# Optimization experiments

Measured on AMD Instinct MI355X. Metric: run time of the kernel, lower is better.

The kernel has to match this reference:

```python
import jax, jax.numpy as jnp
import numpy as np

B, S = 1024, 512
V, E, H, T = 50000, 300, 800, 50


def setup_inputs() -> dict:
    key = jax.random.key(0)
    ks = jax.random.split(key, 8)
    ids = jax.random.randint(ks[0], (B, S), 0, V, dtype=jnp.int64 if jax.config.jax_enable_x64 else jnp.int32)
    return {
        "ids": ids,
        "rho": jax.random.normal(ks[1], (V, E), jnp.float32) * 0.02,
        "alpha": jax.random.normal(ks[2], (T, E), jnp.float32) * 0.02,
        "W1": jax.random.normal(ks[3], (E, H), jnp.float32) * 0.05,
        "b1": jnp.zeros((H,), jnp.float32),
        "Wmu": jax.random.normal(ks[4], (H, T), jnp.float32) * 0.05,
        "bmu": jnp.zeros((T,), jnp.float32),
        "Wlv": jax.random.normal(ks[5], (H, T), jnp.float32) * 0.05,
        "blv": jnp.zeros((T,), jnp.float32),
    }


def reference(ids, rho, alpha, W1, b1, Wmu, bmu, Wlv, blv):
    b, s = ids.shape
    v = rho.shape[0]
    # bag-of-words histogram: scatter-add instead of dense one_hot+reduce_sum
    bows = jnp.zeros((b, v), rho.dtype).at[jnp.arange(b)[:, None], ids].add(1.0)
    # zero out special tokens 1 and 2 (original: x * (1 - sum(one_hot([1,2]))))
    bows = bows.at[:, jnp.array([1, 2])].set(0.0)
    normal_bows = bows / jnp.sum(bows, axis=-1, keepdims=True)
    # encoder (eval mode: dropout is identity)
    x = jnp.einsum('bv,ve->be', normal_bows, rho)
    h = jax.nn.relu(x @ W1 + b1)
    mu_theta = h @ Wmu + bmu
    logsigma_theta = h @ Wlv + blv
    kl_theta = -0.5 * jnp.sum(1.0 + logsigma_theta - mu_theta**2 - jnp.exp(logsigma_theta), axis=-1)
    # reparameterize (eval/inference mode): z = mu
    theta = jax.nn.softmax(mu_theta, axis=-1)  # [B, T]
    beta = jax.nn.softmax(jnp.einsum('te,ve->tv', alpha, rho), axis=-1)  # [T, V]
    lookup = jnp.log(theta @ beta + 1e-5)  # [B, V]
    recon_loss = -jnp.sum(lookup * bows, axis=-1)
    loss = jnp.mean(recon_loss) + jnp.mean(kl_theta)
    return theta, loss
```

## Files before the change

kernel.cpp:

```cpp
#include <hip/hip_runtime.h>
#include <math.h>


#define Bn 1024
#define Sn 512
#define Vn 50000
#define En 300
#define Hn 800
#define Tn 50
#define KP 320
#define BSTR 64
#define W1FRAG_N (50 * 10 * 64 * 8)
#define WFRAG_N  (8 * 25 * 64 * 8)
#define NRANGE 8
#define VRANGE (Vn / NRANGE)

typedef __bf16 bf16x8 __attribute__((ext_vector_type(8)));
typedef float  f32x4  __attribute__((ext_vector_type(4)));

__device__ __forceinline__ float waveReduceSum(float v) {
    #pragma unroll
    for (int off = 32; off > 0; off >>= 1) v += __shfl_xor(v, off, 64);
    return v;
}
__device__ __forceinline__ float waveReduceMax(float v) {
    #pragma unroll
    for (int off = 32; off > 0; off >>= 1) v = fmaxf(v, __shfl_xor(v, off, 64));
    return v;
}
__device__ __forceinline__ unsigned short f2bf(float x) {
    unsigned u = __float_as_uint(x);
    return (unsigned short)((u + 0x7FFFu + ((u >> 16) & 1u)) >> 16);
}
__device__ __forceinline__ float bf_lo(unsigned u) { return __uint_as_float(u << 16); }
__device__ __forceinline__ float bf_hi(unsigned u) { return __uint_as_float(u & 0xFFFF0000u); }

__global__ __launch_bounds__(256) void k0_init(
        const float* __restrict__ alpha, const float* __restrict__ W1,
        const float* __restrict__ Wmu, const float* __restrict__ Wlv,
        unsigned short* __restrict__ bfrag, unsigned short* __restrict__ w1frag,
        unsigned short* __restrict__ wfrag, float* __restrict__ topicsumR,
        float* __restrict__ loss, float* __restrict__ xbar) {
    const int gid = blockIdx.x * 256 + threadIdx.x;
    if (gid < 512) topicsumR[gid] = 0.f;
    if (gid == 520) *loss = 0.f;
    if (gid < Bn * En) xbar[gid] = 0.f;
    if (gid < 4 * 10 * 64 * 8) {
        int j = gid & 7;
        int lane = (gid >> 3) & 63;
        int rest = gid >> 9;
        int kt = rest % 10, w = rest / 10;
        int t = 16 * w + (lane & 15);
        int e = kt * 32 + (lane >> 4) * 8 + j;
        bfrag[gid] = (t < Tn && e < En) ? f2bf(alpha[t * En + e]) : (unsigned short)0;
    }
    if (gid < W1FRAG_N) {
        int j = gid & 7, lane = (gid >> 3) & 63, rest = gid >> 9;
        int kt = rest % 10, nt = rest / 10;
        int e = kt * 32 + (lane >> 4) * 8 + j;
        int hcol = nt * 16 + (lane & 15);
        w1frag[gid] = (e < En) ? f2bf(W1[e * Hn + hcol]) : (unsigned short)0;
    } else {
        int g2 = gid - W1FRAG_N;
        if (g2 < WFRAG_N) {
            int j = g2 & 7, lane = (g2 >> 3) & 63, rest = g2 >> 9;
            int kt = rest % 25, nt = rest / 25;
            int k = kt * 32 + (lane >> 4) * 8 + j;
            int t = (nt & 3) * 16 + (lane & 15);
            float val = 0.f;
            if (t < Tn) val = (nt < 4) ? Wmu[k * Tn + t] : Wlv[k * Tn + t];
            wfrag[g2] = f2bf(val);
        }
    }
}

__global__ __launch_bounds__(256) void k5_cast(
        const float4* __restrict__ rho4, ushort4* __restrict__ rhoh4) {
    const int i = blockIdx.x * 256 + threadIdx.x;
    if (i < Vn * (KP / 4)) {
        int v = i / (KP / 4), s = i - v * (KP / 4);
        ushort4 p = {0, 0, 0, 0};
        if (s < En / 4) {
            float4 r = rho4[v * (En / 4) + s];
            p.x = f2bf(r.x); p.y = f2bf(r.y); p.z = f2bf(r.z); p.w = f2bf(r.w);
        }
        rhoh4[i] = p;
    }
}

__global__ __launch_bounds__(256) void k4_beta(
        const unsigned short* __restrict__ rhoh,
        const unsigned short* __restrict__ bfrag,
        unsigned int* __restrict__ betaU32, float* __restrict__ topicsumR) {
    __shared__ unsigned short trans[16 * 66];
    const int tid = threadIdx.x;
    const int wave = tid >> 6, lane = tid & 63;
    const int quad = lane >> 4, l15 = lane & 15;
    const int v0 = blockIdx.x * 16;

    const unsigned short* arow = rhoh + (size_t)(v0 + l15) * KP + quad * 8;
    f32x4 acc = {0.f, 0.f, 0.f, 0.f};
    #pragma unroll
    for (int kt = 0; kt < 10; ++kt) {
        bf16x8 a = *(const bf16x8*)(arow + kt * 32);
        bf16x8 bv = *(const bf16x8*)(bfrag + ((wave * 10 + kt) * 64 + lane) * 8);
        acc = __builtin_amdgcn_mfma_f32_16x16x32_bf16(a, bv, acc, 0, 0, 0);
    }
    float ts = 0.f;
    #pragma unroll
    for (int r = 0; r < 4; ++r) {
        float ev = expf(acc[r]);
        ts += ev;
        trans[(quad * 4 + r) * 66 + 16 * wave + l15] = f2bf(ev);
    }
    ts += __shfl_xor(ts, 16, 64);
    ts += __shfl_xor(ts, 32, 64);
    const int t = 16 * wave + l15;
    if (lane < 16 && t < Tn)
        atomicAdd(&topicsumR[(blockIdx.x & 7) * 64 + t], ts);
    __syncthreads();
    unsigned int* dst = betaU32 + (size_t)v0 * 32;
    const unsigned int* tr32 = (const unsigned int*)trans;
    for (int i = tid; i < 16 * 32; i += 256)
        dst[i] = tr32[(i >> 5) * 33 + (i & 31)];
}

__global__ __launch_bounds__(256) void k1_tokens_x(
        const int* __restrict__ ids, const unsigned int* __restrict__ rhoh32,
        int* __restrict__ toks, int* __restrict__ cnt,
        float* __restrict__ xbar) {
    __shared__ int sid[Sn];
    __shared__ int sfid[Sn];
    __shared__ int scount, sfull;
    const int blk = blockIdx.x;
    const int r = blk & (NRANGE - 1), b = blk >> 3;
    const int tid = threadIdx.x;
    const int lo = r * VRANGE, hi = lo + VRANGE;
    if (tid == 0) { scount = 0; sfull = 0; }
    __syncthreads();
    #pragma unroll
    for (int s0 = 0; s0 < Sn; s0 += 256) {
        int id = ids[b * Sn + s0 + tid];
        bool val = (id != 1 && id != 2);
        if (val && id >= lo && id < hi) {
            int p = atomicAdd(&scount, 1);
            sid[p] = id;
        }
        if (r == 0 && val) {
            int p = atomicAdd(&sfull, 1);
            sfid[p] = id;
        }
    }
    __syncthreads();
    if (r == 0) {
        const int nf = sfull;
        for (int i = tid; i < nf; i += 256) toks[b * Sn + i] = sfid[i];
        if (tid == 0) cnt[b] = nf;
    }
    const int m = scount;
    if (tid < En / 2 && m > 0) {
        float ax = 0.f, ay = 0.f;
        for (int s = 0; s < m; ++s) {
            unsigned u = rhoh32[sid[s] * (KP / 2) + tid];
            ax += bf_lo(u);
            ay += bf_hi(u);
        }
        atomicAdd(&xbar[b * En + 2 * tid], ax);
        atomicAdd(&xbar[b * En + 2 * tid + 1], ay);
    }
}

__global__ __launch_bounds__(256) void k2a_xcast(
        const float* __restrict__ xbar, const int* __restrict__ cnt,
        unsigned short* __restrict__ xbh) {
    const int gid = blockIdx.x * 256 + threadIdx.x;
    if (gid < Bn * KP) {
        int b = gid / KP, e = gid - b * KP;
        unsigned short out = 0;
        if (e < En) {
            float invn = 1.0f / (float)cnt[b];
            out = f2bf(xbar[b * En + e] * invn);
        }
        xbh[gid] = out;
    }
}

__global__ __launch_bounds__(256) void k2_h(
        const unsigned short* __restrict__ xbh,
        const unsigned short* __restrict__ w1frag,
        const float* __restrict__ b1, unsigned short* __restrict__ hbh) {
    const int tid = threadIdx.x;
    const int wave = tid >> 6, lane = tid & 63;
    const int quad = lane >> 4, l15 = lane & 15;
    const int b0 = blockIdx.x * 16;
    const int nt = blockIdx.y * 4 + wave;
    if (nt >= 50) return;
    const unsigned short* arow = xbh + (size_t)(b0 + l15) * KP + quad * 8;
    f32x4 acc = {0.f, 0.f, 0.f, 0.f};
    #pragma unroll
    for (int kt = 0; kt < 10; ++kt) {
        bf16x8 a = *(const bf16x8*)(arow + kt * 32);
        bf16x8 bv = *(const bf16x8*)(w1frag + ((size_t)(nt * 10 + kt) * 64 + lane) * 8);
        acc = __builtin_amdgcn_mfma_f32_16x16x32_bf16(a, bv, acc, 0, 0, 0);
    }
    const int col = nt * 16 + l15;
    const float bias = b1[col];
    #pragma unroll
    for (int r = 0; r < 4; ++r) {
        int row = b0 + quad * 4 + r;
        hbh[(size_t)row * Hn + col] = f2bf(fmaxf(acc[r] + bias, 0.f));
    }
}

__global__ __launch_bounds__(256) void k3_theta(
        const unsigned short* __restrict__ hbh,
        const unsigned short* __restrict__ wfrag,
        const float* __restrict__ bmu, const float* __restrict__ blv,
        float* __restrict__ theta, float* __restrict__ loss) {
    __shared__ float mlds[16 * 65];
    __shared__ float llds[16 * 65];
    const int tid = threadIdx.x;
    const int wave = tid >> 6, lane = tid & 63;
    const int quad = lane >> 4, l15 = lane & 15;
    const int b0 = blockIdx.x * 16;
    const unsigned short* arow = hbh + (size_t)(b0 + l15) * Hn + quad * 8;
    f32x4 am = {0.f, 0.f, 0.f, 0.f}, al = {0.f, 0.f, 0.f, 0.f};
    #pragma unroll
    for (int kt = 0; kt < 25; ++kt) {
        bf16x8 a  = *(const bf16x8*)(arow + kt * 32);
        bf16x8 bm = *(const bf16x8*)(wfrag + ((size_t)(wave * 25 + kt) * 64 + lane) * 8);
        bf16x8 bl = *(const bf16x8*)(wfrag + ((size_t)((4 + wave) * 25 + kt) * 64 + lane) * 8);
        am = __builtin_amdgcn_mfma_f32_16x16x32_bf16(a, bm, am, 0, 0, 0);
        al = __builtin_amdgcn_mfma_f32_16x16x32_bf16(a, bl, al, 0, 0, 0);
    }
    const int t = wave * 16 + l15;
    const float bm_ = (t < Tn) ? bmu[t] : 0.f;
    const float bl_ = (t < Tn) ? blv[t] : 0.f;
    #pragma unroll
    for (int r = 0; r < 4; ++r) {
        int row = quad * 4 + r;
        mlds[row * 65 + t] = am[r] + bm_;
        llds[row * 65 + t] = al[r] + bl_;
    }
    __syncthreads();
    const int tt = (lane < Tn) ? lane : (Tn - 1);
    const bool act = (lane < Tn);
    float klacc = 0.f;
    #pragma unroll
    for (int k = 0; k < 4; ++k) {
        int row = wave * 4 + k;
        float mu = mlds[row * 65 + tt];
        float lv = llds[row * 65 + tt];
        float m = waveReduceMax(act ? mu : -1e30f);
        float ex = act ? expf(mu - m) : 0.f;
        float ssum = waveReduceSum(ex);
        if (act) theta[(b0 + row) * Tn + lane] = ex / ssum;
        klacc += waveReduceSum(act ? (1.f + lv - mu * mu - expf(lv)) : 0.f);
    }
    if (lane == 0) atomicAdd(loss, -0.5f * klacc * (1.0f / (float)Bn));
}

__global__ __launch_bounds__(256) void k6_recon(
        const int* __restrict__ toks, const int* __restrict__ cnt,
        const float* __restrict__ theta, const float* __restrict__ topicsumR,
        const unsigned short* __restrict__ betaUh, float* __restrict__ loss) {
    __shared__ float sw[Tn];
    __shared__ float swred[4];
    const int b = blockIdx.x, tid = threadIdx.x;
    if (tid < Tn) {
        float z = 0.f;
        #pragma unroll
        for (int j = 0; j < 8; ++j) z += topicsumR[j * 64 + tid];
        sw[tid] = theta[b * Tn + tid] / z;
    }
    __syncthreads();
    float wr[Tn];
    #pragma unroll
    for (int t = 0; t < Tn; ++t) wr[t] = sw[t];
    float lsum = 0.f;
    const int n = cnt[b];
    for (int i = tid; i < n; i += 256) {
        int v = toks[b * Sn + i];
        const uint4* q = (const uint4*)(betaUh + (size_t)v * BSTR);
        float dot = 0.f;
        #pragma unroll
        for (int k = 0; k < 6; ++k) {
            uint4 u = q[k];
            int t = 8 * k;
            dot += wr[t]     * bf_lo(u.x) + wr[t + 1] * bf_hi(u.x);
            dot += wr[t + 2] * bf_lo(u.y) + wr[t + 3] * bf_hi(u.y);
            dot += wr[t + 4] * bf_lo(u.z) + wr[t + 5] * bf_hi(u.z);
            dot += wr[t + 6] * bf_lo(u.w) + wr[t + 7] * bf_hi(u.w);
        }
        unsigned d = ((const unsigned*)q)[24];
        dot += wr[48] * bf_lo(d) + wr[49] * bf_hi(d);
        lsum += logf(dot + 1e-5f);
    }
    float s = waveReduceSum(lsum);
    const int wave = tid >> 6, lane = tid & 63;
    if (lane == 0) swred[wave] = s;
    __syncthreads();
    if (tid == 0) {
        float tot = swred[0] + swred[1] + swred[2] + swred[3];
        atomicAdd(loss, -tot * (1.0f / (float)Bn));
    }
}

extern "C" void kernel_launch(void* const* d_in, const int* in_sizes, int n_in,
                              void* d_out, int out_size, void* d_ws, size_t ws_size,
                              hipStream_t stream) {
    const int*   ids   = (const int*)d_in[0];
    const float* rho   = (const float*)d_in[1];
    const float* alpha = (const float*)d_in[2];
    const float* W1    = (const float*)d_in[3];
    const float* b1    = (const float*)d_in[4];
    const float* Wmu   = (const float*)d_in[5];
    const float* bmu   = (const float*)d_in[6];
    const float* Wlv   = (const float*)d_in[7];
    const float* blv   = (const float*)d_in[8];

    float* theta = (float*)d_out;
    float* loss  = theta + Bn * Tn;

    char* w = (char*)d_ws;
    float* topicsumR = (float*)w;               w += 8 * 64 * 4;
    unsigned short* bfrag = (unsigned short*)w; w += 4 * 10 * 64 * 8 * 2;
    unsigned short* w1frag = (unsigned short*)w; w += (size_t)W1FRAG_N * 2;
    unsigned short* wfrag = (unsigned short*)w;  w += (size_t)WFRAG_N * 2;
    int*   cnt      = (int*)w;                  w += Bn * 4;
    int*   toks     = (int*)w;                  w += Bn * Sn * 4;
    float* xbar     = (float*)w;                w += Bn * En * 4;
    unsigned short* xbh = (unsigned short*)w;   w += (size_t)Bn * KP * 2;
    unsigned short* hbh = (unsigned short*)w;   w += (size_t)Bn * Hn * 2;
    unsigned short* rhoh = (unsigned short*)w;  w += (size_t)Vn * KP * 2;
    unsigned int* betaU32 = (unsigned int*)w;   w += (size_t)Vn * 128;

    const int k0grid = (W1FRAG_N + WFRAG_N + 255) / 256;
    k0_init<<<k0grid, 256, 0, stream>>>(alpha, W1, Wmu, Wlv, bfrag, w1frag,
                                        wfrag, topicsumR, loss, xbar);
    k5_cast<<<(Vn * (KP / 4) + 255) / 256, 256, 0, stream>>>(
        (const float4*)rho, (ushort4*)rhoh);
    k4_beta<<<Vn / 16, 256, 0, stream>>>(rhoh, bfrag, betaU32, topicsumR);
    k1_tokens_x<<<Bn * NRANGE, 256, 0, stream>>>(ids, (const unsigned int*)rhoh,
                                                 toks, cnt, xbar);
    k2a_xcast<<<(Bn * KP + 255) / 256, 256, 0, stream>>>(xbar, cnt, xbh);
    k2_h<<<dim3(64, 13), 256, 0, stream>>>(xbh, w1frag, b1, hbh);
    k3_theta<<<64, 256, 0, stream>>>(hbh, wfrag, bmu, blv, theta, loss);
    k6_recon<<<Bn, 256, 0, stream>>>(toks, cnt, theta, topicsumR,
                                     (const unsigned short*)betaU32, loss);
}
```

Measured before the change: 216.3 us.

## Merge independent kernels into shared launches and fuse x-cast into hidden GEMM

Combines the rho cast with the init kernel, and the beta GEMM with the token/x-accumulation kernel, by partitioning the block index range so independent work shares one launch. The xbar normalisation and bf16 cast are folded into the hidden-layer GEMM through shared memory, which removes the xbh buffer and one launch. This cuts launch overhead and inter-kernel gaps at the cost of heavier blocks and redundant x staging across blockIdx.y. Risk: in the merged launches, the token blocks read rhoh written in the same (earlier) launch, which is fine, but beta and token blocks now contend for the GPU at the same time.

```diff
diff --git a/kernel.cpp b/kernel.cpp
--- a/kernel.cpp
+++ b/kernel.cpp
@@ -14,6 +14,8 @@
 #define WFRAG_N  (8 * 25 * 64 * 8)
 #define NRANGE 8
 #define VRANGE (Vn / NRANGE)
+#define CASTB (Vn * (KP / 4) / 256)
+#define K4B (Vn / 16)
 
 typedef __bf16 bf16x8 __attribute__((ext_vector_type(8)));
 typedef float  f32x4  __attribute__((ext_vector_type(4)));
@@ -35,13 +37,25 @@
 __device__ __forceinline__ float bf_lo(unsigned u) { return __uint_as_float(u << 16); }
 __device__ __forceinline__ float bf_hi(unsigned u) { return __uint_as_float(u & 0xFFFF0000u); }
 
-__global__ __launch_bounds__(256) void k0_init(
+__global__ __launch_bounds__(256) void ka_init(
+        const float4* __restrict__ rho4, ushort4* __restrict__ rhoh4,
         const float* __restrict__ alpha, const float* __restrict__ W1,
         const float* __restrict__ Wmu, const float* __restrict__ Wlv,
         unsigned short* __restrict__ bfrag, unsigned short* __restrict__ w1frag,
         unsigned short* __restrict__ wfrag, float* __restrict__ topicsumR,
         float* __restrict__ loss, float* __restrict__ xbar) {
-    const int gid = blockIdx.x * 256 + threadIdx.x;
+    if (blockIdx.x < CASTB) {
+        const int i = blockIdx.x * 256 + threadIdx.x;
+        int v = i / (KP / 4), s = i - v * (KP / 4);
+        ushort4 p = {0, 0, 0, 0};
+        if (s < En / 4) {
+            float4 r = rho4[v * (En / 4) + s];
+            p.x = f2bf(r.x); p.y = f2bf(r.y); p.z = f2bf(r.z); p.w = f2bf(r.w);
+        }
+        rhoh4[i] = p;
+        return;
+    }
+    const int gid = (blockIdx.x - CASTB) * 256 + threadIdx.x;
     if (gid < 512) topicsumR[gid] = 0.f;
     if (gid == 520) *loss = 0.f;
     if (gid < Bn * En) xbar[gid] = 0.f;
@@ -74,67 +88,51 @@
     }
 }
 
-__global__ __launch_bounds__(256) void k5_cast(
-        const float4* __restrict__ rho4, ushort4* __restrict__ rhoh4) {
-    const int i = blockIdx.x * 256 + threadIdx.x;
-    if (i < Vn * (KP / 4)) {
-        int v = i / (KP / 4), s = i - v * (KP / 4);
-        ushort4 p = {0, 0, 0, 0};
-        if (s < En / 4) {
-            float4 r = rho4[v * (En / 4) + s];
-            p.x = f2bf(r.x); p.y = f2bf(r.y); p.z = f2bf(r.z); p.w = f2bf(r.w);
-        }
-        rhoh4[i] = p;
-    }
-}
-
-__global__ __launch_bounds__(256) void k4_beta(
+__global__ __launch_bounds__(256) void kb_beta_tokens(
         const unsigned short* __restrict__ rhoh,
         const unsigned short* __restrict__ bfrag,
-        unsigned int* __restrict__ betaU32, float* __restrict__ topicsumR) {
+        unsigned int* __restrict__ betaU32, float* __restrict__ topicsumR,
+        const int* __restrict__ ids, int* __restrict__ toks,
+        int* __restrict__ cnt, float* __restrict__ xbar) {
     __shared__ unsigned short trans[16 * 66];
-    const int tid = threadIdx.x;
-    const int wave = tid >> 6, lane = tid & 63;
-    const int quad = lane >> 4, l15 = lane & 15;
-    const int v0 = blockIdx.x * 16;
-
-    const unsigned short* arow = rhoh + (size_t)(v0 + l15) * KP + quad * 8;
-    f32x4 acc = {0.f, 0.f, 0.f, 0.f};
-    #pragma unroll
-    for (int kt = 0; kt < 10; ++kt) {
-        bf16x8 a = *(const bf16x8*)(arow + kt * 32);
-        bf16x8 bv = *(const bf16x8*)(bfrag + ((wave * 10 + kt) * 64 + lane) * 8);
-        acc = __builtin_amdgcn_mfma_f32_16x16x32_bf16(a, bv, acc, 0, 0, 0);
-    }
-    float ts = 0.f;
-    #pragma unroll
-    for (int r = 0; r < 4; ++r) {
-        float ev = expf(acc[r]);
-        ts += ev;
-        trans[(quad * 4 + r) * 66 + 16 * wave + l15] = f2bf(ev);
-    }
-    ts += __shfl_xor(ts, 16, 64);
-    ts += __shfl_xor(ts, 32, 64);
-    const int t = 16 * wave + l15;
-    if (lane < 16 && t < Tn)
-        atomicAdd(&topicsumR[(blockIdx.x & 7) * 64 + t], ts);
-    __syncthreads();
-    unsigned int* dst = betaU32 + (size_t)v0 * 32;
-    const unsigned int* tr32 = (const unsigned int*)trans;
-    for (int i = tid; i < 16 * 32; i += 256)
-        dst[i] = tr32[(i >> 5) * 33 + (i & 31)];
-}
-
-__global__ __launch_bounds__(256) void k1_tokens_x(
-        const int* __restrict__ ids, const unsigned int* __restrict__ rhoh32,
-        int* __restrict__ toks, int* __restrict__ cnt,
-        float* __restrict__ xbar) {
     __shared__ int sid[Sn];
     __shared__ int sfid[Sn];
     __shared__ int scount, sfull;
-    const int blk = blockIdx.x;
+    const int tid = threadIdx.x;
+
+    if (blockIdx.x < K4B) {
+        const int wave = tid >> 6, lane = tid & 63;
+        const int quad = lane >> 4, l15 = lane & 15;
+        const int v0 = blockIdx.x * 16;
+        const unsigned short* arow = rhoh + (size_t)(v0 + l15) * KP + quad * 8;
+        f32x4 acc = {0.f, 0.f, 0.f, 0.f};
+        #pragma unroll
+        for (int kt = 0; kt < 10; ++kt) {
+            bf16x8 a = *(const bf16x8*)(arow + kt * 32);
+            bf16x8 bv = *(const bf16x8*)(bfrag + ((wave * 10 + kt) * 64 + lane) * 8);
+            acc = __builtin_amdgcn_mfma_f32_16x16x32_bf16(a, bv, acc, 0, 0, 0);
+        }
+        float ts = 0.f;
+        #pragma unroll
+        for (int r = 0; r < 4; ++r) {
+            float ev = expf(acc[r]);
+            ts += ev;
+            trans[(quad * 4 + r) * 66 + 16 * wave + l15] = f2bf(ev);
+        }
+        ts += __shfl_xor(ts, 16, 64);
+        ts += __shfl_xor(ts, 32, 64);
+        const int t = 16 * wave + l15;
+        if (lane < 16 && t < Tn)
+            atomicAdd(&topicsumR[(blockIdx.x & 7) * 64 + t], ts);
+        __syncthreads();
+        unsigned int* dst = betaU32 + (size_t)v0 * 32;
+        const unsigned int* tr32 = (const unsigned int*)trans;
+        for (int i = tid; i < 16 * 32; i += 256)
+            dst[i] = tr32[(i >> 5) * 33 + (i & 31)];
+        return;
+    }
+    const int blk = blockIdx.x - K4B;
     const int r = blk & (NRANGE - 1), b = blk >> 3;
-    const int tid = threadIdx.x;
     const int lo = r * VRANGE, hi = lo + VRANGE;
     if (tid == 0) { scount = 0; sfull = 0; }
     __syncthreads();
@@ -158,6 +156,7 @@
         if (tid == 0) cnt[b] = nf;
     }
     const int m = scount;
+    const unsigned int* rhoh32 = (const unsigned int*)rhoh;
     if (tid < En / 2 && m > 0) {
         float ax = 0.f, ay = 0.f;
         for (int s = 0; s < m; ++s) {
@@ -170,45 +169,41 @@
     }
 }
 
-__global__ __launch_bounds__(256) void k2a_xcast(
+__global__ __launch_bounds__(256) void k2m_h(
         const float* __restrict__ xbar, const int* __restrict__ cnt,
-        unsigned short* __restrict__ xbh) {
-    const int gid = blockIdx.x * 256 + threadIdx.x;
-    if (gid < Bn * KP) {
-        int b = gid / KP, e = gid - b * KP;
-        unsigned short out = 0;
-        if (e < En) {
-            float invn = 1.0f / (float)cnt[b];
-            out = f2bf(xbar[b * En + e] * invn);
-        }
-        xbh[gid] = out;
-    }
-}
-
-__global__ __launch_bounds__(256) void k2_h(
-        const unsigned short* __restrict__ xbh,
         const unsigned short* __restrict__ w1frag,
         const float* __restrict__ b1, unsigned short* __restrict__ hbh) {
+    __shared__ unsigned short xs[16 * 328];
+    __shared__ float invn[16];
     const int tid = threadIdx.x;
     const int wave = tid >> 6, lane = tid & 63;
     const int quad = lane >> 4, l15 = lane & 15;
     const int b0 = blockIdx.x * 16;
+    if (tid < 16) invn[tid] = 1.0f / (float)cnt[b0 + tid];
+    __syncthreads();
+    for (int i = tid; i < 16 * KP; i += 256) {
+        int row = i / KP, e = i - row * KP;
+        xs[row * 328 + e] = (e < En) ? f2bf(xbar[(b0 + row) * En + e] * invn[row])
+                                     : (unsigned short)0;
+    }
+    __syncthreads();
     const int nt = blockIdx.y * 4 + wave;
-    if (nt >= 50) return;
-    const unsigned short* arow = xbh + (size_t)(b0 + l15) * KP + quad * 8;
-    f32x4 acc = {0.f, 0.f, 0.f, 0.f};
-    #pragma unroll
-    for (int kt = 0; kt < 10; ++kt) {
-        bf16x8 a = *(const bf16x8*)(arow + kt * 32);
-        bf16x8 bv = *(const bf16x8*)(w1frag + ((size_t)(nt * 10 + kt) * 64 + lane) * 8);
-        acc = __builtin_amdgcn_mfma_f32_16x16x32_bf16(a, bv, acc, 0, 0, 0);
-    }
-    const int col = nt * 16 + l15;
-    const float bias = b1[col];
-    #pragma unroll
-    for (int r = 0; r < 4; ++r) {
-        int row = b0 + quad * 4 + r;
-        hbh[(size_t)row * Hn + col] = f2bf(fmaxf(acc[r] + bias, 0.f));
+    if (nt < 50) {
+        const unsigned short* arow = xs + l15 * 328 + quad * 8;
+        f32x4 acc = {0.f, 0.f, 0.f, 0.f};
+        #pragma unroll
+        for (int kt = 0; kt < 10; ++kt) {
+            bf16x8 a = *(const bf16x8*)(arow + kt * 32);
+            bf16x8 bv = *(const bf16x8*)(w1frag + ((size_t)(nt * 10 + kt) * 64 + lane) * 8);
+            acc = __builtin_amdgcn_mfma_f32_16x16x32_bf16(a, bv, acc, 0, 0, 0);
+        }
+        const int col = nt * 16 + l15;
+        const float bias = b1[col];
+        #pragma unroll
+        for (int r = 0; r < 4; ++r) {
+            int row = b0 + quad * 4 + r;
+            hbh[(size_t)row * Hn + col] = f2bf(fmaxf(acc[r] + bias, 0.f));
+        }
     }
 }
 
@@ -330,21 +325,17 @@
     int*   cnt      = (int*)w;                  w += Bn * 4;
     int*   toks     = (int*)w;                  w += Bn * Sn * 4;
     float* xbar     = (float*)w;                w += Bn * En * 4;
-    unsigned short* xbh = (unsigned short*)w;   w += (size_t)Bn * KP * 2;
     unsigned short* hbh = (unsigned short*)w;   w += (size_t)Bn * Hn * 2;
     unsigned short* rhoh = (unsigned short*)w;  w += (size_t)Vn * KP * 2;
     unsigned int* betaU32 = (unsigned int*)w;   w += (size_t)Vn * 128;
 
     const int k0grid = (W1FRAG_N + WFRAG_N + 255) / 256;
-    k0_init<<<k0grid, 256, 0, stream>>>(alpha, W1, Wmu, Wlv, bfrag, w1frag,
-                                        wfrag, topicsumR, loss, xbar);
-    k5_cast<<<(Vn * (KP / 4) + 255) / 256, 256, 0, stream>>>(
-        (const float4*)rho, (ushort4*)rhoh);
-    k4_beta<<<Vn / 16, 256, 0, stream>>>(rhoh, bfrag, betaU32, topicsumR);
-    k1_tokens_x<<<Bn * NRANGE, 256, 0, stream>>>(ids, (const unsigned int*)rhoh,
-                                                 toks, cnt, xbar);
-    k2a_xcast<<<(Bn * KP + 255) / 256, 256, 0, stream>>>(xbar, cnt, xbh);
-    k2_h<<<dim3(64, 13), 256, 0, stream>>>(xbh, w1frag, b1, hbh);
+    ka_init<<<CASTB + k0grid, 256, 0, stream>>>(
+        (const float4*)rho, (ushort4*)rhoh, alpha, W1, Wmu, Wlv,
+        bfrag, w1frag, wfrag, topicsumR, loss, xbar);
+    kb_beta_tokens<<<K4B + Bn * NRANGE, 256, 0, stream>>>(
+        rhoh, bfrag, betaU32, topicsumR, ids, toks, cnt, xbar);
+    k2m_h<<<dim3(64, 13), 256, 0, stream>>>(xbar, cnt, w1frag, b1, hbh);
     k3_theta<<<64, 256, 0, stream>>>(hbh, wfrag, bmu, blv, theta, loss);
     k6_recon<<<Bn, 256, 0, stream>>>(toks, cnt, theta, topicsumR,
                                      (const unsigned short*)betaU32, loss);
```

Result: faster. 208.4 us (-3.7%).
